# Kernel optimization log

Hardware: AMD Instinct MI355X
Metric: run time of the kernel (lower is better)

The kernel has to match this reference:

```python
import jax, jax.numpy as jnp
import numpy as np

ALPHA = 0.05
MAX_ITER = 200
TOL = 0.01
N = 64
M = 1
BATCH = 262144


def setup_inputs() -> dict:
    key = jax.random.key(0)
    pred_cost = jax.random.normal(key, (BATCH, N), dtype=jnp.float32)
    # constraint data (fixed buffers, match init_kwargs)
    A = np.ones((M, N), dtype=np.float32)
    b = np.full((M,), 32.0, dtype=np.float32)
    lb = np.zeros((N,), dtype=np.float32)
    ub = np.ones((N,), dtype=np.float32)
    # SVD-based pseudoinverse factors for equality projection
    U, s, VT = np.linalg.svd(A, full_matrices=False)
    s_inv = np.where(s >= 1e-6, 1.0 / s, 0.0).astype(np.float32)
    return {
        "pred_cost": pred_cost,
        "A": jnp.asarray(A),
        "b": jnp.asarray(b),
        "lb": jnp.asarray(lb),
        "ub": jnp.asarray(ub),
        "V": jnp.asarray(VT.T.astype(np.float32)),   # (n, m)
        "UT": jnp.asarray(U.T.astype(np.float32)),   # (m, m)
        "s_inv": jnp.asarray(s_inv),                 # (m,)
    }


def _project_box(z, lb, ub):
    return jnp.clip(z, lb, ub)


def _project_equality(w, A, b, V, UT, s_inv):
    # w: (B, n). residual r = A w^T - b, correction = V diag(s_inv) U^T r
    r = w @ A.T - b                      # (B, m)
    corr = ((r @ UT.T) * s_inv) @ V.T    # (B, n)
    return w - corr


def _dys_step(z, cost, A, b, lb, ub, V, UT, s_inv):
    x = _project_box(z, lb, ub)
    grad = cost + ALPHA * x              # grad of regularized objective
    y = _project_equality(2.0 * x - z - ALPHA * grad, A, b, V, UT, s_inv)
    return z - x + y


def _run_to_convergence(cost, A, b, lb, ub, V, UT, s_inv):
    lb_safe = jnp.where(jnp.isfinite(lb), lb, 0.0)
    ub_safe = jnp.where(jnp.isfinite(ub), ub, 1.0)
    z0 = jax.random.uniform(jax.random.key(1), cost.shape, dtype=cost.dtype)
    z0 = z0 * (ub_safe - lb_safe) + lb_safe

    def cond(state):
        i, z, diff = state
        return jnp.logical_and(i < MAX_ITER, diff > TOL)

    def body(state):
        i, z, _ = state
        z_new = _dys_step(z, cost, A, b, lb, ub, V, UT, s_inv)
        diff = jnp.max(jnp.linalg.norm(z_new - z, axis=1))
        return (i + 1, z_new, diff)

    _, z, _ = jax.lax.while_loop(cond, body, (jnp.int32(0), z0, jnp.float32(1e30)))
    return z


def reference(pred_cost, A, b, lb, ub, V, UT, s_inv):
    cost = pred_cost  # minimize=True
    # no-grad fixed-point iterations
    z = jax.lax.stop_gradient(
        _run_to_convergence(jax.lax.stop_gradient(cost), A, b, lb, ub, V, UT, s_inv)
    )
    # training branch: one differentiable DYS step (JFB), then box projection
    z = _dys_step(z, cost, A, b, lb, ub, V, UT, s_inv)
    sol = _project_box(z, lb, ub)
    return sol
```

## Files before the change

kernel.cpp:

```cpp
#include <hip/hip_runtime.h>
#include <cstdint>


#ifndef JAX_PARTITIONABLE
#define JAX_PARTITIONABLE 1
#endif

#define BATCHN 262144
#define MAXIT  200
#define ROWS_PER_WAVE 16
#define NWAVES (BATCHN / ROWS_PER_WAVE)
#define PROBE_ROWS 4096
#define PROBE_WAVES (PROBE_ROWS / ROWS_PER_WAVE)

#define K1 0.9975f
#define K2 1.9975f

__device__ __forceinline__ void tf2x32(uint32_t x0, uint32_t x1,
                                       uint32_t& o0, uint32_t& o1) {
  const uint32_t k0 = 0u, k1 = 1u;
  const uint32_t k2 = 0x1BD11BDAu ^ k0 ^ k1;
  x0 += k0; x1 += k1;
#define TFR(r) { x0 += x1; x1 = (x1 << (r)) | (x1 >> (32 - (r))); x1 ^= x0; }
  TFR(13) TFR(15) TFR(26) TFR(6)   x0 += k1; x1 += k2 + 1u;
  TFR(17) TFR(29) TFR(16) TFR(24)  x0 += k2; x1 += k0 + 2u;
  TFR(13) TFR(15) TFR(26) TFR(6)   x0 += k0; x1 += k1 + 3u;
  TFR(17) TFR(29) TFR(16) TFR(24)  x0 += k1; x1 += k2 + 4u;
  TFR(13) TFR(15) TFR(26) TFR(6)   x0 += k2; x1 += k0 + 5u;
#undef TFR
  o0 = x0; o1 = x1;
}

__device__ __forceinline__ float z0_at(uint32_t f) {
  uint32_t b;
#if JAX_PARTITIONABLE
  uint32_t o0, o1;
  tf2x32(0u, f, o0, o1);
  b = o0 ^ o1;
#else
  const uint32_t H = 8388608u;
  uint32_t lo = (f < H) ? f : (f - H);
  uint32_t o0, o1;
  tf2x32(lo, lo + H, o0, o1);
  b = (f < H) ? o0 : o1;
#endif
  return __uint_as_float((b >> 9) | 0x3f800000u) - 1.0f;
}

__device__ __forceinline__ float reduce4(float v) {
  v += __shfl_xor(v, 1);
  v += __shfl_xor(v, 2);
  return v;
}

__device__ __forceinline__ float tsum16(const float* a) {
  float b0 = a[0] + a[1],  b1 = a[2] + a[3],  b2 = a[4] + a[5],
        b3 = a[6] + a[7],  b4 = a[8] + a[9],  b5 = a[10] + a[11],
        b6 = a[12] + a[13], b7 = a[14] + a[15];
  float c0 = b0 + b1, c1 = b2 + b3, c2 = b4 + b5, c3 = b6 + b7;
  return (c0 + c1) + (c2 + c3);
}

template <bool WANT>
__device__ __forceinline__ float u_iter(float u[16], const float ac[16],
                                        float& C, float& Chi, float& R) {
  float m[16];
#pragma unroll
  for (int j = 0; j < 16; ++j) m[j] = __builtin_amdgcn_fmed3f(u[j], C, Chi);
  float Sm = reduce4(tsum16(m));
  float Sx = __builtin_fmaf(-64.0f, C, Sm);
  float t    = __builtin_fmaf(K2, Sx, -R);
  float corr = __builtin_fmaf(t, 0.015625f, -0.5f);
  R = (R - Sx) + 32.0f;
  float Cn = __builtin_fmaf(K1, C, corr);
  float dC = Cn - C;
  C = Cn; Chi = Cn + 1.0f;
  float dsa = 0.0f, dsb = 0.0f;
#pragma unroll
  for (int j = 0; j < 16; ++j) {
    float un = __builtin_fmaf(K1, m[j], -ac[j]);
    if (WANT) {
      float d = (un - u[j]) - dC;
      if (j & 1) dsb = __builtin_fmaf(d, d, dsb);
      else       dsa = __builtin_fmaf(d, d, dsa);
    }
    u[j] = un;
  }
  if (!WANT) return 0.0f;
  return reduce4(dsa + dsb);
}

__device__ __forceinline__ void load_ac(const float* __restrict__ cost,
                                        int base, float ac[16]) {
#pragma unroll
  for (int k = 0; k < 4; ++k) {
    const float4 c = *(const float4*)(cost + base + 4 * k);
    ac[4 * k + 0] = 0.05f * c.x; ac[4 * k + 1] = 0.05f * c.y;
    ac[4 * k + 2] = 0.05f * c.z; ac[4 * k + 3] = 0.05f * c.w;
  }
}

__device__ __forceinline__ void init_state(const float* __restrict__ cost,
                                           int base, float ac[16], float u[16],
                                           float& C, float& Chi, float& R) {
  load_ac(cost, base, ac);
  float r0 = 0.0f;
#pragma unroll
  for (int j = 0; j < 16; ++j) {
    u[j] = z0_at((uint32_t)(base + j));
    r0 += u[j] + ac[j];
  }
  C = 0.0f; Chi = 1.0f;
  R = reduce4(r0);
}

__global__ __launch_bounds__(256) void dys_probe(
    const float* __restrict__ cost, int* __restrict__ Tsample) {
  const int lane = threadIdx.x & 63;
  const int gw = blockIdx.x * 4 + (threadIdx.x >> 6);
  const int base = (gw * ROWS_PER_WAVE + (lane >> 2)) * 64 + (lane & 3) * 16;

  float ac[16], u[16], C, Chi, R;
  init_state(cost, base, ac, u, C, Chi, R);

  int ib = MAXIT;
  for (int i = 1; i <= MAXIT; ++i) {
    float ds = u_iter<true>(u, ac, C, Chi, R);
    if (__all(ds <= 1.0e-4f)) { ib = i; break; }
  }
  if (lane == 0) atomicMax(Tsample, ib);
}

__global__ __launch_bounds__(256) void dys_pass1(
    const float* __restrict__ cost, const int* __restrict__ Tsample,
    int* __restrict__ Tglob, int* __restrict__ TrArr,
    float* __restrict__ zst) {
  const int lane = threadIdx.x & 63;
  const int gw = blockIdx.x * 4 + (threadIdx.x >> 6);
  const int base = (gw * ROWS_PER_WAVE + (lane >> 2)) * 64 + (lane & 3) * 16;

  float ac[16], u[16], C, Chi, R;
  init_state(cost, base, ac, u, C, Chi, R);

  const int Ts = *Tsample;
  const int P = (Ts > 3) ? (Ts - 3) : 0;

  for (int i = 0; i < P; ++i) u_iter<false>(u, ac, C, Chi, R);

  int ib = MAXIT;
  for (int i = P + 1; i <= MAXIT; ++i) {
    float ds = u_iter<true>(u, ac, C, Chi, R);
    if (__all(ds <= 1.0e-4f)) { ib = i; break; }
  }

#pragma unroll
  for (int k = 0; k < 4; ++k) {
    float4 zq;
    zq.x = u[4 * k + 0] - C; zq.y = u[4 * k + 1] - C;
    zq.z = u[4 * k + 2] - C; zq.w = u[4 * k + 3] - C;
    *(float4*)(zst + base + 4 * k) = zq;
  }
  if (lane == 0) {
    TrArr[gw] = ib;
    atomicMax(Tglob, ib);
  }
}

__global__ __launch_bounds__(256) void dys_pass2(
    const float* __restrict__ cost, const int* __restrict__ Tglob,
    const int* __restrict__ TrArr, const float* __restrict__ zst,
    float* __restrict__ out) {
  const int lane = threadIdx.x & 63;
  const int gw = blockIdx.x * 4 + (threadIdx.x >> 6);
  const int base = (gw * ROWS_PER_WAVE + (lane >> 2)) * 64 + (lane & 3) * 16;

  float ac[16], u[16];
  load_ac(cost, base, ac);
  float r0 = 0.0f;
#pragma unroll
  for (int k = 0; k < 4; ++k) {
    const float4 zq = *(const float4*)(zst + base + 4 * k);
    u[4 * k + 0] = zq.x; u[4 * k + 1] = zq.y;
    u[4 * k + 2] = zq.z; u[4 * k + 3] = zq.w;
  }
#pragma unroll
  for (int j = 0; j < 16; ++j) r0 += u[j] + ac[j];
  float C = 0.0f, Chi = 1.0f;
  float R = reduce4(r0);

  const int T = *Tglob;
  const int ib = TrArr[gw];

  for (int i = ib; i <= T; ++i) u_iter<false>(u, ac, C, Chi, R);

#pragma unroll
  for (int k = 0; k < 4; ++k) {
    float4 o;
    o.x = __builtin_amdgcn_fmed3f(u[4 * k + 0] - C, 0.0f, 1.0f);
    o.y = __builtin_amdgcn_fmed3f(u[4 * k + 1] - C, 0.0f, 1.0f);
    o.z = __builtin_amdgcn_fmed3f(u[4 * k + 2] - C, 0.0f, 1.0f);
    o.w = __builtin_amdgcn_fmed3f(u[4 * k + 3] - C, 0.0f, 1.0f);
    *(float4*)(out + base + 4 * k) = o;
  }
}

extern "C" void kernel_launch(void* const* d_in, const int* in_sizes, int n_in,
                              void* d_out, int out_size, void* d_ws,
                              size_t ws_size, hipStream_t stream) {
  const float* cost = (const float*)d_in[0];
  float* out = (float*)d_out;

  int* Tglob   = (int*)d_ws;
  int* Tsample = (int*)d_ws + 1;
  const size_t TR_OFF = 1024;
  const size_t Z_OFF  = TR_OFF + (size_t)NWAVES * sizeof(int);
  int*   TrArr = (int*)((char*)d_ws + TR_OFF);
  float* zst   = (float*)((char*)d_ws + Z_OFF);

  hipMemsetAsync(d_ws, 0, 8, stream);

  dim3 block(256);
  dys_probe<<<dim3(PROBE_WAVES / 4), block, 0, stream>>>(cost, Tsample);
  dys_pass1<<<dim3(NWAVES / 4), block, 0, stream>>>(cost, Tsample, Tglob,
                                                    TrArr, zst);
  dys_pass2<<<dim3(NWAVES / 4), block, 0, stream>>>(cost, Tglob, TrArr, zst,
                                                    out);
}
```

Measured before the change: 417.7 us.

## Rescale DYS state by 20 and map each row to two lanes

The state is rescaled by 20 so the cost enters the update without a multiply and the box upper bound becomes CC+20. Each row is now handled by two lanes with 32 elements each instead of four lanes with 16, which cuts the cross-lane shuffles per reduction from two to one. The convergence norm is computed algebraically from sums of d and d² plus the shift change, and the threshold is scaled to match. Larger per-thread arrays raise register pressure, which the launch bounds of 4 try to contain, and the probe now samples twice as many rows.

```diff
diff --git a/kernel.cpp b/kernel.cpp
--- a/kernel.cpp
+++ b/kernel.cpp
@@ -8,10 +8,10 @@
 
 #define BATCHN 262144
 #define MAXIT  200
-#define ROWS_PER_WAVE 16
-#define NWAVES (BATCHN / ROWS_PER_WAVE)
-#define PROBE_ROWS 4096
-#define PROBE_WAVES (PROBE_ROWS / ROWS_PER_WAVE)
+#define RPW    32
+#define NWAVES (BATCHN / RPW)
+#define PROBE_ROWS 8192
+#define PROBE_WAVES (PROBE_ROWS / RPW)
 
 #define K1 0.9975f
 #define K2 1.9975f
@@ -47,117 +47,142 @@
   return __uint_as_float((b >> 9) | 0x3f800000u) - 1.0f;
 }
 
-__device__ __forceinline__ float reduce4(float v) {
-  v += __shfl_xor(v, 1);
-  v += __shfl_xor(v, 2);
-  return v;
-}
-
-__device__ __forceinline__ float tsum16(const float* a) {
-  float b0 = a[0] + a[1],  b1 = a[2] + a[3],  b2 = a[4] + a[5],
-        b3 = a[6] + a[7],  b4 = a[8] + a[9],  b5 = a[10] + a[11],
-        b6 = a[12] + a[13], b7 = a[14] + a[15];
-  float c0 = b0 + b1, c1 = b2 + b3, c2 = b4 + b5, c3 = b6 + b7;
-  return (c0 + c1) + (c2 + c3);
-}
-
-template <bool WANT>
-__device__ __forceinline__ float u_iter(float u[16], const float ac[16],
-                                        float& C, float& Chi, float& R) {
-  float m[16];
-#pragma unroll
-  for (int j = 0; j < 16; ++j) m[j] = __builtin_amdgcn_fmed3f(u[j], C, Chi);
-  float Sm = reduce4(tsum16(m));
-  float Sx = __builtin_fmaf(-64.0f, C, Sm);
-  float t    = __builtin_fmaf(K2, Sx, -R);
-  float corr = __builtin_fmaf(t, 0.015625f, -0.5f);
+__device__ __forceinline__ void fast_iter(float U[32], const float c[32],
+                                          float& CC, float& R) {
+  const float Ch = CC + 20.0f;
+  float g[8];
+#pragma unroll
+  for (int q = 0; q < 8; ++q) {
+    float m0 = __builtin_amdgcn_fmed3f(U[4 * q + 0], CC, Ch);
+    float m1 = __builtin_amdgcn_fmed3f(U[4 * q + 1], CC, Ch);
+    float m2 = __builtin_amdgcn_fmed3f(U[4 * q + 2], CC, Ch);
+    float m3 = __builtin_amdgcn_fmed3f(U[4 * q + 3], CC, Ch);
+    U[4 * q + 0] = __builtin_fmaf(K1, m0, -c[4 * q + 0]);
+    U[4 * q + 1] = __builtin_fmaf(K1, m1, -c[4 * q + 1]);
+    U[4 * q + 2] = __builtin_fmaf(K1, m2, -c[4 * q + 2]);
+    U[4 * q + 3] = __builtin_fmaf(K1, m3, -c[4 * q + 3]);
+    g[q] = (m0 + m1) + (m2 + m3);
+  }
+  float s = ((g[0] + g[1]) + (g[2] + g[3])) + ((g[4] + g[5]) + (g[6] + g[7]));
+  s += __shfl_xor(s, 1);
+  float Sx = 0.05f * __builtin_fmaf(-64.0f, CC, s);
+  float t  = __builtin_fmaf(K2, Sx, -R);
+  float corr20 = __builtin_fmaf(t, 0.3125f, -10.0f);
   R = (R - Sx) + 32.0f;
-  float Cn = __builtin_fmaf(K1, C, corr);
-  float dC = Cn - C;
-  C = Cn; Chi = Cn + 1.0f;
-  float dsa = 0.0f, dsb = 0.0f;
-#pragma unroll
-  for (int j = 0; j < 16; ++j) {
-    float un = __builtin_fmaf(K1, m[j], -ac[j]);
-    if (WANT) {
-      float d = (un - u[j]) - dC;
-      if (j & 1) dsb = __builtin_fmaf(d, d, dsb);
-      else       dsa = __builtin_fmaf(d, d, dsa);
+  CC = __builtin_fmaf(K1, CC, corr20);
+}
+
+__device__ __forceinline__ float chk_iter(float U[32], const float c[32],
+                                          float& CC, float& R) {
+  const float Ch = CC + 20.0f;
+  float g[8];
+  float q1 = 0.0f, q2 = 0.0f;
+#pragma unroll
+  for (int q = 0; q < 8; ++q) {
+    float m0 = __builtin_amdgcn_fmed3f(U[4 * q + 0], CC, Ch);
+    float m1 = __builtin_amdgcn_fmed3f(U[4 * q + 1], CC, Ch);
+    float m2 = __builtin_amdgcn_fmed3f(U[4 * q + 2], CC, Ch);
+    float m3 = __builtin_amdgcn_fmed3f(U[4 * q + 3], CC, Ch);
+    g[q] = (m0 + m1) + (m2 + m3);
+#pragma unroll
+    for (int e = 0; e < 4; ++e) {
+      int j = 4 * q + e;
+      float m = (e == 0) ? m0 : (e == 1) ? m1 : (e == 2) ? m2 : m3;
+      float un = __builtin_fmaf(K1, m, -c[j]);
+      float d = un - U[j];
+      q1 += d;
+      q2 = __builtin_fmaf(d, d, q2);
+      U[j] = un;
     }
-    u[j] = un;
-  }
-  if (!WANT) return 0.0f;
-  return reduce4(dsa + dsb);
-}
-
-__device__ __forceinline__ void load_ac(const float* __restrict__ cost,
-                                        int base, float ac[16]) {
-#pragma unroll
-  for (int k = 0; k < 4; ++k) {
-    const float4 c = *(const float4*)(cost + base + 4 * k);
-    ac[4 * k + 0] = 0.05f * c.x; ac[4 * k + 1] = 0.05f * c.y;
-    ac[4 * k + 2] = 0.05f * c.z; ac[4 * k + 3] = 0.05f * c.w;
+  }
+  float s = ((g[0] + g[1]) + (g[2] + g[3])) + ((g[4] + g[5]) + (g[6] + g[7]));
+  s += __shfl_xor(s, 1);
+  float Sx = 0.05f * __builtin_fmaf(-64.0f, CC, s);
+  float t  = __builtin_fmaf(K2, Sx, -R);
+  float corr20 = __builtin_fmaf(t, 0.3125f, -10.0f);
+  R = (R - Sx) + 32.0f;
+  float CCn = __builtin_fmaf(K1, CC, corr20);
+  float dCC = CCn - CC;
+  CC = CCn;
+  q1 += __shfl_xor(q1, 1);
+  q2 += __shfl_xor(q2, 1);
+  float a = __builtin_fmaf(64.0f, dCC, -2.0f * q1);
+  return __builtin_fmaf(dCC, a, q2);
+}
+
+__device__ __forceinline__ void load_c(const float* __restrict__ cost,
+                                       int base, float c[32]) {
+#pragma unroll
+  for (int k = 0; k < 8; ++k) {
+    const float4 cq = *(const float4*)(cost + base + 4 * k);
+    c[4 * k + 0] = cq.x; c[4 * k + 1] = cq.y;
+    c[4 * k + 2] = cq.z; c[4 * k + 3] = cq.w;
   }
 }
 
 __device__ __forceinline__ void init_state(const float* __restrict__ cost,
-                                           int base, float ac[16], float u[16],
-                                           float& C, float& Chi, float& R) {
-  load_ac(cost, base, ac);
-  float r0 = 0.0f;
-#pragma unroll
-  for (int j = 0; j < 16; ++j) {
-    u[j] = z0_at((uint32_t)(base + j));
-    r0 += u[j] + ac[j];
-  }
-  C = 0.0f; Chi = 1.0f;
-  R = reduce4(r0);
-}
-
-__global__ __launch_bounds__(256) void dys_probe(
+                                           int base, float c[32], float U[32],
+                                           float& CC, float& R) {
+  load_c(cost, base, c);
+  float r = 0.0f;
+#pragma unroll
+  for (int j = 0; j < 32; ++j) {
+    float z0 = z0_at((uint32_t)(base + j));
+    U[j] = 20.0f * z0;
+    r = __builtin_fmaf(0.05f, c[j], r + z0);
+  }
+  r += __shfl_xor(r, 1);
+  R = r;
+  CC = 0.0f;
+}
+
+__global__ __launch_bounds__(256, 4) void dys_probe(
     const float* __restrict__ cost, int* __restrict__ Tsample) {
   const int lane = threadIdx.x & 63;
   const int gw = blockIdx.x * 4 + (threadIdx.x >> 6);
-  const int base = (gw * ROWS_PER_WAVE + (lane >> 2)) * 64 + (lane & 3) * 16;
-
-  float ac[16], u[16], C, Chi, R;
-  init_state(cost, base, ac, u, C, Chi, R);
+  const int base = (gw * RPW + (lane >> 1)) * 64 + (lane & 1) * 32;
+
+  float c[32], U[32], CC, R;
+  init_state(cost, base, c, U, CC, R);
 
   int ib = MAXIT;
   for (int i = 1; i <= MAXIT; ++i) {
-    float ds = u_iter<true>(u, ac, C, Chi, R);
-    if (__all(ds <= 1.0e-4f)) { ib = i; break; }
+    float ds = chk_iter(U, c, CC, R);
+    if (__all(ds <= 0.04f)) { ib = i; break; }
   }
   if (lane == 0) atomicMax(Tsample, ib);
 }
 
-__global__ __launch_bounds__(256) void dys_pass1(
+__global__ __launch_bounds__(256, 4) void dys_pass1(
     const float* __restrict__ cost, const int* __restrict__ Tsample,
     int* __restrict__ Tglob, int* __restrict__ TrArr,
     float* __restrict__ zst) {
   const int lane = threadIdx.x & 63;
   const int gw = blockIdx.x * 4 + (threadIdx.x >> 6);
-  const int base = (gw * ROWS_PER_WAVE + (lane >> 2)) * 64 + (lane & 3) * 16;
-
-  float ac[16], u[16], C, Chi, R;
-  init_state(cost, base, ac, u, C, Chi, R);
+  const int base = (gw * RPW + (lane >> 1)) * 64 + (lane & 1) * 32;
+
+  float c[32], U[32], CC, R;
+  init_state(cost, base, c, U, CC, R);
 
   const int Ts = *Tsample;
-  const int P = (Ts > 3) ? (Ts - 3) : 0;
-
-  for (int i = 0; i < P; ++i) u_iter<false>(u, ac, C, Chi, R);
+  const int P = (Ts > 2) ? (Ts - 2) : 0;
+
+  for (int i = 0; i < P; ++i) fast_iter(U, c, CC, R);
 
   int ib = MAXIT;
   for (int i = P + 1; i <= MAXIT; ++i) {
-    float ds = u_iter<true>(u, ac, C, Chi, R);
-    if (__all(ds <= 1.0e-4f)) { ib = i; break; }
-  }
-
-#pragma unroll
-  for (int k = 0; k < 4; ++k) {
+    float ds = chk_iter(U, c, CC, R);
+    if (__all(ds <= 0.04f)) { ib = i; break; }
+  }
+
+  const float CC05 = 0.05f * CC;
+#pragma unroll
+  for (int k = 0; k < 8; ++k) {
     float4 zq;
-    zq.x = u[4 * k + 0] - C; zq.y = u[4 * k + 1] - C;
-    zq.z = u[4 * k + 2] - C; zq.w = u[4 * k + 3] - C;
+    zq.x = __builtin_fmaf(0.05f, U[4 * k + 0], -CC05);
+    zq.y = __builtin_fmaf(0.05f, U[4 * k + 1], -CC05);
+    zq.z = __builtin_fmaf(0.05f, U[4 * k + 2], -CC05);
+    zq.w = __builtin_fmaf(0.05f, U[4 * k + 3], -CC05);
     *(float4*)(zst + base + 4 * k) = zq;
   }
   if (lane == 0) {
@@ -166,40 +191,46 @@
   }
 }
 
-__global__ __launch_bounds__(256) void dys_pass2(
+__global__ __launch_bounds__(256, 4) void dys_pass2(
     const float* __restrict__ cost, const int* __restrict__ Tglob,
     const int* __restrict__ TrArr, const float* __restrict__ zst,
     float* __restrict__ out) {
   const int lane = threadIdx.x & 63;
   const int gw = blockIdx.x * 4 + (threadIdx.x >> 6);
-  const int base = (gw * ROWS_PER_WAVE + (lane >> 2)) * 64 + (lane & 3) * 16;
-
-  float ac[16], u[16];
-  load_ac(cost, base, ac);
-  float r0 = 0.0f;
-#pragma unroll
-  for (int k = 0; k < 4; ++k) {
+  const int base = (gw * RPW + (lane >> 1)) * 64 + (lane & 1) * 32;
+
+  float c[32], U[32];
+  load_c(cost, base, c);
+  float r = 0.0f;
+#pragma unroll
+  for (int k = 0; k < 8; ++k) {
     const float4 zq = *(const float4*)(zst + base + 4 * k);
-    u[4 * k + 0] = zq.x; u[4 * k + 1] = zq.y;
-    u[4 * k + 2] = zq.z; u[4 * k + 3] = zq.w;
-  }
-#pragma unroll
-  for (int j = 0; j < 16; ++j) r0 += u[j] + ac[j];
-  float C = 0.0f, Chi = 1.0f;
-  float R = reduce4(r0);
+    U[4 * k + 0] = 20.0f * zq.x; U[4 * k + 1] = 20.0f * zq.y;
+    U[4 * k + 2] = 20.0f * zq.z; U[4 * k + 3] = 20.0f * zq.w;
+    r += (zq.x + zq.y) + (zq.z + zq.w);
+  }
+#pragma unroll
+  for (int j = 0; j < 32; ++j) r = __builtin_fmaf(0.05f, c[j], r);
+  float CC = 0.0f;
+  float R = r + __shfl_xor(r, 1);
 
   const int T = *Tglob;
   const int ib = TrArr[gw];
 
-  for (int i = ib; i <= T; ++i) u_iter<false>(u, ac, C, Chi, R);
-
-#pragma unroll
-  for (int k = 0; k < 4; ++k) {
+  for (int i = ib; i <= T; ++i) fast_iter(U, c, CC, R);
+
+  const float CC05 = 0.05f * CC;
+#pragma unroll
+  for (int k = 0; k < 8; ++k) {
     float4 o;
-    o.x = __builtin_amdgcn_fmed3f(u[4 * k + 0] - C, 0.0f, 1.0f);
-    o.y = __builtin_amdgcn_fmed3f(u[4 * k + 1] - C, 0.0f, 1.0f);
-    o.z = __builtin_amdgcn_fmed3f(u[4 * k + 2] - C, 0.0f, 1.0f);
-    o.w = __builtin_amdgcn_fmed3f(u[4 * k + 3] - C, 0.0f, 1.0f);
+    o.x = __builtin_amdgcn_fmed3f(
+        __builtin_fmaf(0.05f, U[4 * k + 0], -CC05), 0.0f, 1.0f);
+    o.y = __builtin_amdgcn_fmed3f(
+        __builtin_fmaf(0.05f, U[4 * k + 1], -CC05), 0.0f, 1.0f);
+    o.z = __builtin_amdgcn_fmed3f(
+        __builtin_fmaf(0.05f, U[4 * k + 2], -CC05), 0.0f, 1.0f);
+    o.w = __builtin_amdgcn_fmed3f(
+        __builtin_fmaf(0.05f, U[4 * k + 3], -CC05), 0.0f, 1.0f);
     *(float4*)(out + base + 4 * k) = o;
   }
 }
```

Result: slower. 448.5 us (+7.4%).

## Simplify DYS iteration recurrence, cheapen convergence check, store midpoint state in fp16

Applied to the files above, without the earlier changes.

Rewrites the per-row scalar recurrence so each iteration carries only the previous clipped sum instead of a running residual, which removes several dependent scalar ops from the hot loop. The convergence check now expands the squared norm algebraically into two reductions (sum of d and sum of d^2), so the per-element subtraction of dC goes away. The intermediate z state passed between pass1 and pass2 is packed to fp16, halving that memory traffic. The probe sample size is doubled and the unchecked prefix is extended by one iteration. The fp16 storage and the expanded norm add rounding error, which could change iteration counts or output accuracy.

```diff
diff --git a/kernel.cpp b/kernel.cpp
--- a/kernel.cpp
+++ b/kernel.cpp
@@ -8,13 +8,17 @@
 
 #define BATCHN 262144
 #define MAXIT  200
-#define ROWS_PER_WAVE 16
-#define NWAVES (BATCHN / ROWS_PER_WAVE)
-#define PROBE_ROWS 4096
-#define PROBE_WAVES (PROBE_ROWS / ROWS_PER_WAVE)
-
-#define K1 0.9975f
-#define K2 1.9975f
+#define RPW    16
+#define NWAVES (BATCHN / RPW)
+#define PROBE_ROWS 8192
+#define PROBE_WAVES (PROBE_ROWS / RPW)
+
+#define K1f 0.9975f
+#define KAf ((float)((1.0 + (double)K1f) / 64.0))
+#define KBf ((float)(((double)K1f) / 64.0))
+#define RINVf ((float)(1.0 / (double)K1f))
+
+typedef __fp16 h2v __attribute__((ext_vector_type(2)));
 
 __device__ __forceinline__ void tf2x32(uint32_t x0, uint32_t x1,
                                        uint32_t& o0, uint32_t& o1) {
@@ -61,71 +65,85 @@
   return (c0 + c1) + (c2 + c3);
 }
 
-template <bool WANT>
-__device__ __forceinline__ float u_iter(float u[16], const float ac[16],
-                                        float& C, float& Chi, float& R) {
+__device__ __forceinline__ void fast_iter(float u[16], const float ac[16],
+                                          float& C, float& Chi, float& Smp) {
   float m[16];
 #pragma unroll
   for (int j = 0; j < 16; ++j) m[j] = __builtin_amdgcn_fmed3f(u[j], C, Chi);
-  float Sm = reduce4(tsum16(m));
-  float Sx = __builtin_fmaf(-64.0f, C, Sm);
-  float t    = __builtin_fmaf(K2, Sx, -R);
-  float corr = __builtin_fmaf(t, 0.015625f, -0.5f);
-  R = (R - Sx) + 32.0f;
-  float Cn = __builtin_fmaf(K1, C, corr);
+  float s = tsum16(m);
+#pragma unroll
+  for (int j = 0; j < 16; ++j) u[j] = __builtin_fmaf(K1f, m[j], -ac[j]);
+  s = reduce4(s);
+  float Cn = __builtin_fmaf(KAf, s, __builtin_fmaf(-KBf, Smp, -0.5f));
+  Smp = s;
+  C = Cn;
+  Chi = Cn + 1.0f;
+}
+
+__device__ __forceinline__ float chk_iter(float u[16], const float ac[16],
+                                          float& C, float& Chi, float& Smp) {
+  float m[16];
+#pragma unroll
+  for (int j = 0; j < 16; ++j) m[j] = __builtin_amdgcn_fmed3f(u[j], C, Chi);
+  float s = tsum16(m);
+  float q1 = 0.0f, q2 = 0.0f;
+#pragma unroll
+  for (int j = 0; j < 16; ++j) {
+    float un = __builtin_fmaf(K1f, m[j], -ac[j]);
+    float d = un - u[j];
+    q1 += d;
+    q2 = __builtin_fmaf(d, d, q2);
+    u[j] = un;
+  }
+  s = reduce4(s);
+  float Cn = __builtin_fmaf(KAf, s, __builtin_fmaf(-KBf, Smp, -0.5f));
   float dC = Cn - C;
-  C = Cn; Chi = Cn + 1.0f;
-  float dsa = 0.0f, dsb = 0.0f;
-#pragma unroll
-  for (int j = 0; j < 16; ++j) {
-    float un = __builtin_fmaf(K1, m[j], -ac[j]);
-    if (WANT) {
-      float d = (un - u[j]) - dC;
-      if (j & 1) dsb = __builtin_fmaf(d, d, dsb);
-      else       dsa = __builtin_fmaf(d, d, dsa);
-    }
-    u[j] = un;
-  }
-  if (!WANT) return 0.0f;
-  return reduce4(dsa + dsb);
+  Smp = s;
+  C = Cn;
+  Chi = Cn + 1.0f;
+  q1 = reduce4(q1);
+  q2 = reduce4(q2);
+  float a = __builtin_fmaf(64.0f, dC, -2.0f * q1);
+  return __builtin_fmaf(dC, a, q2);
 }
 
 __device__ __forceinline__ void load_ac(const float* __restrict__ cost,
                                         int base, float ac[16]) {
 #pragma unroll
   for (int k = 0; k < 4; ++k) {
-    const float4 c = *(const float4*)(cost + base + 4 * k);
-    ac[4 * k + 0] = 0.05f * c.x; ac[4 * k + 1] = 0.05f * c.y;
-    ac[4 * k + 2] = 0.05f * c.z; ac[4 * k + 3] = 0.05f * c.w;
+    const float4 cq = *(const float4*)(cost + base + 4 * k);
+    ac[4 * k + 0] = 0.05f * cq.x; ac[4 * k + 1] = 0.05f * cq.y;
+    ac[4 * k + 2] = 0.05f * cq.z; ac[4 * k + 3] = 0.05f * cq.w;
   }
 }
 
 __device__ __forceinline__ void init_state(const float* __restrict__ cost,
                                            int base, float ac[16], float u[16],
-                                           float& C, float& Chi, float& R) {
+                                           float& C, float& Chi, float& Smp) {
   load_ac(cost, base, ac);
-  float r0 = 0.0f;
+  float r = 0.0f;
 #pragma unroll
   for (int j = 0; j < 16; ++j) {
     u[j] = z0_at((uint32_t)(base + j));
-    r0 += u[j] + ac[j];
-  }
+    r += u[j] + ac[j];
+  }
+  float R = reduce4(r);
   C = 0.0f; Chi = 1.0f;
-  R = reduce4(r0);
+  Smp = R * RINVf;
 }
 
 __global__ __launch_bounds__(256) void dys_probe(
     const float* __restrict__ cost, int* __restrict__ Tsample) {
   const int lane = threadIdx.x & 63;
   const int gw = blockIdx.x * 4 + (threadIdx.x >> 6);
-  const int base = (gw * ROWS_PER_WAVE + (lane >> 2)) * 64 + (lane & 3) * 16;
-
-  float ac[16], u[16], C, Chi, R;
-  init_state(cost, base, ac, u, C, Chi, R);
+  const int base = (gw * RPW + (lane >> 2)) * 64 + (lane & 3) * 16;
+
+  float ac[16], u[16], C, Chi, Smp;
+  init_state(cost, base, ac, u, C, Chi, Smp);
 
   int ib = MAXIT;
   for (int i = 1; i <= MAXIT; ++i) {
-    float ds = u_iter<true>(u, ac, C, Chi, R);
+    float ds = chk_iter(u, ac, C, Chi, Smp);
     if (__all(ds <= 1.0e-4f)) { ib = i; break; }
   }
   if (lane == 0) atomicMax(Tsample, ib);
@@ -134,32 +152,36 @@
 __global__ __launch_bounds__(256) void dys_pass1(
     const float* __restrict__ cost, const int* __restrict__ Tsample,
     int* __restrict__ Tglob, int* __restrict__ TrArr,
-    float* __restrict__ zst) {
+    uint32_t* __restrict__ zh) {
   const int lane = threadIdx.x & 63;
   const int gw = blockIdx.x * 4 + (threadIdx.x >> 6);
-  const int base = (gw * ROWS_PER_WAVE + (lane >> 2)) * 64 + (lane & 3) * 16;
-
-  float ac[16], u[16], C, Chi, R;
-  init_state(cost, base, ac, u, C, Chi, R);
+  const int base = (gw * RPW + (lane >> 2)) * 64 + (lane & 3) * 16;
+
+  float ac[16], u[16], C, Chi, Smp;
+  init_state(cost, base, ac, u, C, Chi, Smp);
 
   const int Ts = *Tsample;
-  const int P = (Ts > 3) ? (Ts - 3) : 0;
-
-  for (int i = 0; i < P; ++i) u_iter<false>(u, ac, C, Chi, R);
+  const int P = (Ts > 2) ? (Ts - 2) : 0;
+
+  for (int i = 0; i < P; ++i) fast_iter(u, ac, C, Chi, Smp);
 
   int ib = MAXIT;
   for (int i = P + 1; i <= MAXIT; ++i) {
-    float ds = u_iter<true>(u, ac, C, Chi, R);
+    float ds = chk_iter(u, ac, C, Chi, Smp);
     if (__all(ds <= 1.0e-4f)) { ib = i; break; }
   }
 
-#pragma unroll
-  for (int k = 0; k < 4; ++k) {
-    float4 zq;
-    zq.x = u[4 * k + 0] - C; zq.y = u[4 * k + 1] - C;
-    zq.z = u[4 * k + 2] - C; zq.w = u[4 * k + 3] - C;
-    *(float4*)(zst + base + 4 * k) = zq;
-  }
+  uint32_t pk[8];
+#pragma unroll
+  for (int j = 0; j < 8; ++j) {
+    float zx = u[2 * j] - C;
+    float zy = u[2 * j + 1] - C;
+    h2v h = __builtin_amdgcn_cvt_pkrtz(zx, zy);
+    pk[j] = *(uint32_t*)&h;
+  }
+  const int ub = base >> 1;
+  *(uint4*)(zh + ub)     = make_uint4(pk[0], pk[1], pk[2], pk[3]);
+  *(uint4*)(zh + ub + 4) = make_uint4(pk[4], pk[5], pk[6], pk[7]);
   if (lane == 0) {
     TrArr[gw] = ib;
     atomicMax(Tglob, ib);
@@ -168,30 +190,34 @@
 
 __global__ __launch_bounds__(256) void dys_pass2(
     const float* __restrict__ cost, const int* __restrict__ Tglob,
-    const int* __restrict__ TrArr, const float* __restrict__ zst,
+    const int* __restrict__ TrArr, const uint32_t* __restrict__ zh,
     float* __restrict__ out) {
   const int lane = threadIdx.x & 63;
   const int gw = blockIdx.x * 4 + (threadIdx.x >> 6);
-  const int base = (gw * ROWS_PER_WAVE + (lane >> 2)) * 64 + (lane & 3) * 16;
+  const int base = (gw * RPW + (lane >> 2)) * 64 + (lane & 3) * 16;
 
   float ac[16], u[16];
   load_ac(cost, base, ac);
-  float r0 = 0.0f;
-#pragma unroll
-  for (int k = 0; k < 4; ++k) {
-    const float4 zq = *(const float4*)(zst + base + 4 * k);
-    u[4 * k + 0] = zq.x; u[4 * k + 1] = zq.y;
-    u[4 * k + 2] = zq.z; u[4 * k + 3] = zq.w;
-  }
-#pragma unroll
-  for (int j = 0; j < 16; ++j) r0 += u[j] + ac[j];
+  const int ub = base >> 1;
+  const uint4 pa = *(const uint4*)(zh + ub);
+  const uint4 pb = *(const uint4*)(zh + ub + 4);
+  uint32_t pk[8] = {pa.x, pa.y, pa.z, pa.w, pb.x, pb.y, pb.z, pb.w};
+  float r = 0.0f;
+#pragma unroll
+  for (int j = 0; j < 8; ++j) {
+    h2v h = *(h2v*)&pk[j];
+    u[2 * j]     = (float)h.x;
+    u[2 * j + 1] = (float)h.y;
+    r += ((float)h.x + ac[2 * j]) + ((float)h.y + ac[2 * j + 1]);
+  }
+  float R = reduce4(r);
   float C = 0.0f, Chi = 1.0f;
-  float R = reduce4(r0);
+  float Smp = R * RINVf;
 
   const int T = *Tglob;
   const int ib = TrArr[gw];
 
-  for (int i = ib; i <= T; ++i) u_iter<false>(u, ac, C, Chi, R);
+  for (int i = ib; i <= T; ++i) fast_iter(u, ac, C, Chi, Smp);
 
 #pragma unroll
   for (int k = 0; k < 4; ++k) {
@@ -214,15 +240,15 @@
   int* Tsample = (int*)d_ws + 1;
   const size_t TR_OFF = 1024;
   const size_t Z_OFF  = TR_OFF + (size_t)NWAVES * sizeof(int);
-  int*   TrArr = (int*)((char*)d_ws + TR_OFF);
-  float* zst   = (float*)((char*)d_ws + Z_OFF);
-
-  hipMemsetAsync(d_ws, 0, 8, stream);
+  int*      TrArr = (int*)((char*)d_ws + TR_OFF);
+  uint32_t* zh    = (uint32_t*)((char*)d_ws + Z_OFF);
+
+  (void)hipMemsetAsync(d_ws, 0, 8, stream);
 
   dim3 block(256);
   dys_probe<<<dim3(PROBE_WAVES / 4), block, 0, stream>>>(cost, Tsample);
   dys_pass1<<<dim3(NWAVES / 4), block, 0, stream>>>(cost, Tsample, Tglob,
-                                                    TrArr, zst);
-  dys_pass2<<<dim3(NWAVES / 4), block, 0, stream>>>(cost, Tglob, TrArr, zst,
+                                                    TrArr, zh);
+  dys_pass2<<<dim3(NWAVES / 4), block, 0, stream>>>(cost, Tglob, TrArr, zh,
                                                     out);
 }
```

Result: no change. 414.1 us (-0.9%).
